# Optimization experiments

Hardware: AMD Instinct MI355X
Metric: run time of the kernel (lower is better)

Reference implementation:

```python
import jax, jax.numpy as jnp
import numpy as np

N_NODES = 50000
N_EDGES = 1600000
IN_C = 64
OUT_C = 64
N_CLASSES = 45


def setup_inputs() -> dict:
    key = jax.random.key(0)
    ks = jax.random.split(key, 12)

    def lin(k, i, o):
        return jax.random.normal(k, (i, o), jnp.float32) / np.float32(np.sqrt(i))

    return dict(
        x=jax.random.normal(ks[0], (N_NODES, IN_C), jnp.float32),
        edge_index=jax.random.randint(ks[1], (2, N_EDGES), 0, N_NODES, dtype=jnp.int32),
        W_z=lin(ks[2], IN_C, OUT_C), b_z=jnp.zeros((OUT_C,), jnp.float32),
        Wl_z=lin(ks[3], 2 * OUT_C, OUT_C), bl_z=jnp.zeros((OUT_C,), jnp.float32),
        W_r=lin(ks[4], IN_C, OUT_C), b_r=jnp.zeros((OUT_C,), jnp.float32),
        Wl_r=lin(ks[5], 2 * OUT_C, OUT_C), bl_r=jnp.zeros((OUT_C,), jnp.float32),
        W_h=lin(ks[6], IN_C, OUT_C), b_h=jnp.zeros((OUT_C,), jnp.float32),
        Wl_h=lin(ks[7], 2 * OUT_C, OUT_C), bl_h=jnp.zeros((OUT_C,), jnp.float32),
        W_out=lin(ks[8], OUT_C, N_CLASSES), b_out=jnp.zeros((N_CLASSES,), jnp.float32),
    )


def _gcn(x, W, b, src, dst, dinv):
    # GCNConv with improved self-loops (fill value 2.0):
    # out = D^{-1/2} (A + 2I) D^{-1/2} X W + b, with deg = in_degree + 2
    xw = x @ W                                   # [N, OUT_C]
    norm = dinv[src] * dinv[dst]                 # [E]
    agg = jax.ops.segment_sum(norm[:, None] * xw[src], dst, num_segments=N_NODES)
    agg = agg + (2.0 * dinv * dinv)[:, None] * xw  # self-loop contribution
    return agg + b


def reference(x, edge_index, W_z, b_z, Wl_z, bl_z, W_r, b_r, Wl_r, bl_r,
              W_h, b_h, Wl_h, bl_h, W_out, b_out):
    src, dst = edge_index[0], edge_index[1]
    deg = jax.ops.segment_sum(jnp.ones((N_EDGES,), jnp.float32), dst,
                              num_segments=N_NODES) + 2.0
    dinv = jax.lax.rsqrt(deg)

    # TGCN cell with H0 = 0 (no prior hidden state passed)
    H = jnp.zeros((N_NODES, OUT_C), x.dtype)
    Z = jax.nn.sigmoid(
        jnp.concatenate([_gcn(x, W_z, b_z, src, dst, dinv), H], axis=1) @ Wl_z + bl_z)
    R = jax.nn.sigmoid(
        jnp.concatenate([_gcn(x, W_r, b_r, src, dst, dinv), H], axis=1) @ Wl_r + bl_r)
    H_tilde = jnp.tanh(
        jnp.concatenate([_gcn(x, W_h, b_h, src, dst, dinv), H * R], axis=1) @ Wl_h + bl_h)
    H = Z * H + (1.0 - Z) * H_tilde

    # relu + linear readout to 45 classes
    return jax.nn.relu(H) @ W_out + b_out
```

## Files before the change

kernel.cpp:

```cpp
#include <hip/hip_runtime.h>

#define N_NODES 50000
#define N_EDGES 1600000
#define NB 782
#define NBB 256
#define CHUNK 6250
#define CAP 2560
#define SCAP 3072
#define ZROW 50000
#define NTILES 3125

typedef unsigned short ushort_t;
typedef _Float16 v8h __attribute__((ext_vector_type(8)));
typedef _Float16 v4h __attribute__((ext_vector_type(4)));
typedef float f32x4_t __attribute__((ext_vector_type(4)));

__global__ __launch_bounds__(256) void k_binw(
    const int* __restrict__ ei, int* __restrict__ gcur, int* __restrict__ bins,
    const float* __restrict__ Wz, const float* __restrict__ bz,
    const float* __restrict__ Wlz, const float* __restrict__ blz,
    const float* __restrict__ Wh, const float* __restrict__ bh,
    const float* __restrict__ Wlh, const float* __restrict__ blh,
    const float* __restrict__ Wout, float* __restrict__ B2f,
    _Float16* __restrict__ Bzh, _Float16* __restrict__ Bwo) {
  __shared__ int arena[8320];
  int tid = threadIdx.x, blk = blockIdx.x;
  if (blk < NBB) {
    int* h    = arena;
    int* segb = arena + NB;
    int* pk   = arena + 2 * NB;
    for (int i = tid; i < NB; i += 256) h[i] = 0;
    __syncthreads();
    const int2* s2 = (const int2*)(ei + blk * CHUNK);
    const int2* d2 = (const int2*)(ei + N_EDGES + blk * CHUNK);
    for (int i = tid; i < CHUNK / 2; i += 256) {
      int2 s = s2[i];
      int2 d = d2[i];
      pk[2 * i]     = s.x | ((d.x & 63) << 16) | ((d.x >> 6) << 22);
      pk[2 * i + 1] = s.y | ((d.y & 63) << 16) | ((d.y >> 6) << 22);
      atomicAdd(&h[d.x >> 6], 1);
      atomicAdd(&h[d.y >> 6], 1);
    }
    __syncthreads();
    for (int b = tid; b < NB; b += 256) {
      int c = h[b];
      segb[b] = c ? atomicAdd(&gcur[b], c) : 0;
      h[b] = 0;
    }
    __syncthreads();
    for (int i = tid; i < CHUNK; i += 256) {
      int v = pk[i];
      int b = (unsigned)v >> 22;
      int p = atomicAdd(&h[b], 1);
      bins[b * CAP + segb[b] + p] = v & 0x3FFFFF;
    }
  } else {
    int wblk = blk - NBB;
    float* A  = (float*)arena;
    float* Bm = (float*)(arena + 4160);
    bool zpath = wblk < 4;
    const float* Wsrc = zpath ? Wz : Wh;
    const float* Lsrc = zpath ? Wlz : Wlh;
    for (int idx = tid; idx < 4096; idx += 256) {
      A[(idx >> 6) * 65 + (idx & 63)] = Wsrc[idx];
      Bm[(idx >> 6) * 65 + (idx & 63)] = Lsrc[idx];
    }
    __syncthreads();
    int lane = (tid >> 1) & 63;
    int j0 = (tid & 1) * 4;
    int ks = (tid >> 7) & 1;
    int k0 = ks * 32 + ((lane >> 4) << 3) + j0;
    int col = (wblk & 3) * 16 + (lane & 15);
    float a0 = 0.f, a1 = 0.f, a2 = 0.f, a3 = 0.f;
    for (int q = 0; q < 64; ++q) {
      float bv = Bm[q * 65 + col];
      a0 = fmaf(A[k0 * 65 + q], bv, a0);
      a1 = fmaf(A[(k0 + 1) * 65 + q], bv, a1);
      a2 = fmaf(A[(k0 + 2) * 65 + q], bv, a2);
      a3 = fmaf(A[(k0 + 3) * 65 + q], bv, a3);
    }
    int tb = wblk * 1024 + tid * 4;
    v4h o; o[0] = (_Float16)a0; o[1] = (_Float16)a1;
    o[2] = (_Float16)a2; o[3] = (_Float16)a3;
    *(v4h*)(Bzh + tb) = o;
    if ((wblk == 0 || wblk == 4) && tid < 64) {
      float v = zpath ? blz[tid] : blh[tid];
      const float* bb = zpath ? bz : bh;
      for (int q = 0; q < 64; ++q) v = fmaf(bb[q], Bm[q * 65 + tid], v);
      B2f[tid * 2 + (zpath ? 0 : 1)] = v;
    }
    if (wblk == 1) {
      for (int e2 = 0; e2 < 12; ++e2) {
        int t2 = tid * 12 + e2;
        int ln = (t2 >> 3) & 63, j = t2 & 7;
        int ntile = t2 >> 10, ks2 = (t2 >> 9) & 1;
        int n = ntile * 16 + (ln & 15);
        int k = ks2 * 32 + ((ln >> 4) << 3) + j;
        Bwo[t2] = (_Float16)((n < 45) ? Wout[k * 45 + n] : 0.f);
      }
    }
  }
}

__global__ __launch_bounds__(256, 4) void k_sort(
    const int* __restrict__ bins, const int* __restrict__ gcur,
    const float* __restrict__ x,
    ushort_t* __restrict__ srcp, int2* __restrict__ rowiv,
    float* __restrict__ dinv, _Float16* __restrict__ xp) {
  __shared__ int dg[64], lo[64], cur[64];
  __shared__ float sdin[64];
  __shared__ int Tsh;
  __shared__ ushort_t buf[8192];
  int tid = threadIdx.x, b = blockIdx.x;
  int start = b * CAP, end = start + gcur[b];
  if (tid < 64) dg[tid] = 0;
  __syncthreads();
  for (int i = start + tid; i < end; i += 256)
    atomicAdd(&dg[bins[i] >> 16], 1);
  __syncthreads();
  int pdv = 0;
  if (tid < 64) { pdv = (dg[tid] + 7) & ~7; lo[tid] = pdv; }
  __syncthreads();
  for (int off = 1; off < 64; off <<= 1) {
    int u = 0;
    if (tid < 64 && tid >= off) u = lo[tid - off];
    __syncthreads();
    if (tid < 64) lo[tid] += u;
    __syncthreads();
  }
  int ex = 0;
  if (tid < 64) {
    ex = lo[tid] - pdv;
    cur[tid] = ex;
    if (tid == 63) Tsh = lo[63];
  }
  __syncthreads();
  int T = Tsh;
  int base = b * SCAP;
  for (int i = tid; i < T; i += 256) buf[i] = (ushort_t)ZROW;
  __syncthreads();
  for (int i = start + tid; i < end; i += 256) {
    int v = bins[i];
    int dl = v >> 16;
    int p = atomicAdd(&cur[dl], 1);
    buf[p] = (ushort_t)(v & 0xFFFF);
  }
  __syncthreads();
  for (int i = tid; i < T; i += 256) srcp[base + i] = buf[i];
  if (tid < 64) {
    int v = b * 64 + tid;
    if (v < N_NODES) {
      rowiv[v] = make_int2(base + ex, pdv);
      float dv = rsqrtf((float)dg[tid] + 2.0f);
      dinv[v] = dv;
      sdin[tid] = dv;
    } else {
      sdin[tid] = 0.f;
    }
  }
  __syncthreads();
  int nb64 = b * 4096;
  for (int idx = tid; idx < 4096; idx += 256) {
    int v = b * 64 + (idx >> 6);
    if (v < N_NODES) xp[nb64 + idx] = (_Float16)(sdin[idx >> 6] * x[nb64 + idx]);
  }
  if (b == 0 && tid < 64) xp[ZROW * 64 + tid] = (_Float16)0.f;
}

__global__ __launch_bounds__(256) void k_agg(
    const ushort_t* __restrict__ srcp, const int2* __restrict__ rowiv,
    const float* __restrict__ dinv, const _Float16* __restrict__ xp,
    _Float16* __restrict__ sxg) {
  int tid = threadIdx.x;
  int lane = tid & 63;
  int grp = lane >> 4;
  int sub = lane & 15;
  int chOff = sub << 2;
  int w = blockIdx.x * 4 + (tid >> 6);
  int nw = gridDim.x * 4;
  for (int v = w; v < N_NODES; v += nw) {
    int vu = __builtin_amdgcn_readfirstlane(v);
    int2 ri = rowiv[vu];
    int beg = ri.x, pd = ri.y;
    float aA0=0.f,aA1=0.f,aA2=0.f,aA3=0.f, aB0=0.f,aB1=0.f,aB2=0.f,aB3=0.f;
    float aC0=0.f,aC1=0.f,aC2=0.f,aC3=0.f, aD0=0.f,aD1=0.f,aD2=0.f,aD3=0.f;
    for (int e = beg; e < beg + pd; e += 64) {
      int rem = beg + pd - e;
      int m = rem < 64 ? rem : 64;
      int sv = (lane < m) ? (int)srcp[e + lane] : ZROW;
      int t = 0;
      for (; t + 16 <= m; t += 16) {
        int sA = __builtin_amdgcn_ds_bpermute((t + grp) << 2, sv);
        int sB = __builtin_amdgcn_ds_bpermute((t + 4 + grp) << 2, sv);
        int sC = __builtin_amdgcn_ds_bpermute((t + 8 + grp) << 2, sv);
        int sD = __builtin_amdgcn_ds_bpermute((t + 12 + grp) << 2, sv);
        v4h rA = *(const v4h*)(xp + (sA << 6) + chOff);
        v4h rB = *(const v4h*)(xp + (sB << 6) + chOff);
        v4h rC = *(const v4h*)(xp + (sC << 6) + chOff);
        v4h rD = *(const v4h*)(xp + (sD << 6) + chOff);
        aA0 += (float)rA[0]; aA1 += (float)rA[1];
        aA2 += (float)rA[2]; aA3 += (float)rA[3];
        aB0 += (float)rB[0]; aB1 += (float)rB[1];
        aB2 += (float)rB[2]; aB3 += (float)rB[3];
        aC0 += (float)rC[0]; aC1 += (float)rC[1];
        aC2 += (float)rC[2]; aC3 += (float)rC[3];
        aD0 += (float)rD[0]; aD1 += (float)rD[1];
        aD2 += (float)rD[2]; aD3 += (float)rD[3];
      }
      if (t < m) {
        int sA = __builtin_amdgcn_ds_bpermute((t + grp) << 2, sv);
        int sB = __builtin_amdgcn_ds_bpermute((t + 4 + grp) << 2, sv);
        v4h rA = *(const v4h*)(xp + (sA << 6) + chOff);
        v4h rB = *(const v4h*)(xp + (sB << 6) + chOff);
        aA0 += (float)rA[0]; aA1 += (float)rA[1];
        aA2 += (float)rA[2]; aA3 += (float)rA[3];
        aB0 += (float)rB[0]; aB1 += (float)rB[1];
        aB2 += (float)rB[2]; aB3 += (float)rB[3];
      }
    }
    float a0 = (aA0 + aB0) + (aC0 + aD0);
    float a1 = (aA1 + aB1) + (aC1 + aD1);
    float a2 = (aA2 + aB2) + (aC2 + aD2);
    float a3 = (aA3 + aB3) + (aC3 + aD3);
    a0 += __shfl_xor(a0, 16); a1 += __shfl_xor(a1, 16);
    a2 += __shfl_xor(a2, 16); a3 += __shfl_xor(a3, 16);
    a0 += __shfl_xor(a0, 32); a1 += __shfl_xor(a1, 32);
    a2 += __shfl_xor(a2, 32); a3 += __shfl_xor(a3, 32);
    if (lane < 16) {
      float dv = dinv[vu];
      v4h self = *(const v4h*)(xp + (vu << 6) + chOff);
      v4h o;
      o[0] = (_Float16)(dv * a0 + 2.f * dv * (float)self[0]);
      o[1] = (_Float16)(dv * a1 + 2.f * dv * (float)self[1]);
      o[2] = (_Float16)(dv * a2 + 2.f * dv * (float)self[2]);
      o[3] = (_Float16)(dv * a3 + 2.f * dv * (float)self[3]);
      *(v4h*)(sxg + (vu << 6) + chOff) = o;
    }
  }
}

__global__ __launch_bounds__(256) void k_cell(
    const _Float16* __restrict__ sxg, const _Float16* __restrict__ Bzh,
    const _Float16* __restrict__ Bwo, const float2* __restrict__ B2,
    const float* __restrict__ bout, float* __restrict__ out) {
  __shared__ __align__(16) _Float16 tbuf[4][16][72];
  int tid = threadIdx.x;
  int lane = tid & 63, wv = tid >> 6;
  int l15 = lane & 15, quad = lane >> 4;
  int tile = blockIdx.x * 4 + wv;
  if (tile >= NTILES) return;

  v8h bzf[8][2], bwf[3][2];
  #pragma unroll
  for (int t = 0; t < 8; ++t)
    #pragma unroll
    for (int ks = 0; ks < 2; ++ks)
      bzf[t][ks] = *(const v8h*)(Bzh + (((t * 2 + ks) * 64 + lane) << 3));
  #pragma unroll
  for (int t = 0; t < 3; ++t)
    #pragma unroll
    for (int ks = 0; ks < 2; ++ks)
      bwf[t][ks] = *(const v8h*)(Bwo + (((t * 2 + ks) * 64 + lane) << 3));
  float zb[4], hb[4], ob[3];
  #pragma unroll
  for (int t = 0; t < 4; ++t) {
    float2 bb = B2[t * 16 + l15];
    zb[t] = bb.x; hb[t] = bb.y;
  }
  #pragma unroll
  for (int t = 0; t < 3; ++t) {
    int c = t * 16 + l15;
    ob[t] = (c < 45) ? bout[c] : 0.f;
  }

  const _Float16* ar = sxg + (tile * 16 + l15) * 64 + quad * 8;
  v8h a0 = *(const v8h*)ar;
  v8h a1 = *(const v8h*)(ar + 32);

  f32x4_t accz[8];
  #pragma unroll
  for (int t = 0; t < 8; ++t) {
    f32x4_t c4 = {0.f, 0.f, 0.f, 0.f};
    c4 = __builtin_amdgcn_mfma_f32_16x16x32_f16(a0, bzf[t][0], c4, 0, 0, 0);
    c4 = __builtin_amdgcn_mfma_f32_16x16x32_f16(a1, bzf[t][1], c4, 0, 0, 0);
    accz[t] = c4;
  }

  #pragma unroll
  for (int t = 0; t < 4; ++t) {
    #pragma unroll
    for (int r = 0; r < 4; ++r) {
      float zv = accz[t][r] + zb[t];
      float hv = accz[t + 4][r] + hb[t];
      float Z = 1.f / (1.f + __expf(-zv));
      float tt = fminf(15.f, fmaxf(-15.f, hv));
      float e2 = __expf(-2.f * tt);
      float Th = (1.f - e2) / (1.f + e2);
      tbuf[wv][quad * 4 + r][t * 16 + l15] = (_Float16)fmaxf((1.f - Z) * Th, 0.f);
    }
  }
  __asm__ volatile("s_waitcnt lgkmcnt(0)" ::: "memory");

  v8h p0 = *(const v8h*)&tbuf[wv][l15][quad * 8];
  v8h p1 = *(const v8h*)&tbuf[wv][l15][32 + quad * 8];

  #pragma unroll
  for (int t = 0; t < 3; ++t) {
    f32x4_t o4 = {0.f, 0.f, 0.f, 0.f};
    o4 = __builtin_amdgcn_mfma_f32_16x16x32_f16(p0, bwf[t][0], o4, 0, 0, 0);
    o4 = __builtin_amdgcn_mfma_f32_16x16x32_f16(p1, bwf[t][1], o4, 0, 0, 0);
    int c = t * 16 + l15;
    if (c < 45) {
      #pragma unroll
      for (int r = 0; r < 4; ++r)
        out[(tile * 16 + quad * 4 + r) * 45 + c] = o4[r] + ob[t];
    }
  }
}

extern "C" void kernel_launch(void* const* d_in, const int* in_sizes, int n_in,
                              void* d_out, int out_size, void* d_ws, size_t ws_size,
                              hipStream_t stream) {
  const float* x    = (const float*)d_in[0];
  const int*   ei   = (const int*)d_in[1];
  const float* Wz   = (const float*)d_in[2];
  const float* bz   = (const float*)d_in[3];
  const float* Wlz  = (const float*)d_in[4];
  const float* blz  = (const float*)d_in[5];
  const float* Wh   = (const float*)d_in[10];
  const float* bh   = (const float*)d_in[11];
  const float* Wlh  = (const float*)d_in[12];
  const float* blh  = (const float*)d_in[13];
  const float* Wout = (const float*)d_in[14];
  const float* bout = (const float*)d_in[15];
  float* out = (float*)d_out;

  char* w = (char*)d_ws;
  int*      bins  = (int*)(w + 0);
  _Float16* sxg   = (_Float16*)(w + 0);
  int*      gcur  = (int*)(w + 8007680);
  ushort_t* srcp  = (ushort_t*)(w + 8010816);
  int2*     rowiv = (int2*)(w + 12815424);
  float*    dinv  = (float*)(w + 13215424);
  float2*   B2    = (float2*)(w + 13415424);
  _Float16* Bzh   = (_Float16*)(w + 13415936);
  _Float16* Bwo   = (_Float16*)(w + 13432320);
  _Float16* xp    = (_Float16*)(w + 13438464);

  hipMemsetAsync(gcur, 0, NB * sizeof(int), stream);
  k_binw <<<NBB + 8, 256, 0, stream>>>(ei, gcur, bins, Wz, bz, Wlz, blz,
                                       Wh, bh, Wlh, blh, Wout,
                                       (float*)B2, Bzh, Bwo);
  k_sort <<<NB, 256, 0, stream>>>(bins, gcur, x, srcp, rowiv, dinv, xp);
  k_agg  <<<2048, 256, 0, stream>>>(srcp, rowiv, dinv, xp, sxg);
  k_cell <<<NB, 256, 0, stream>>>(sxg, Bzh, Bwo, B2, bout, out);
}
```

Baseline: 161.6 us.

## Fuse neighbor aggregation into the GRU cell kernel and vectorize x scaling

```diff
diff --git a/kernel.cpp b/kernel.cpp
--- a/kernel.cpp
+++ b/kernel.cpp
@@ -159,41 +159,68 @@
     }
   }
   __syncthreads();
+  const float4* x4 = (const float4*)x;
+  int base4 = b * 1024;
   int nb64 = b * 4096;
-  for (int idx = tid; idx < 4096; idx += 256) {
-    int v = b * 64 + (idx >> 6);
-    if (v < N_NODES) xp[nb64 + idx] = (_Float16)(sdin[idx >> 6] * x[nb64 + idx]);
+  for (int idx = tid; idx < 1024; idx += 256) {
+    int row = idx >> 4;
+    int v = b * 64 + row;
+    if (v < N_NODES) {
+      float4 xv = x4[base4 + idx];
+      float s = sdin[row];
+      v4h o;
+      o[0] = (_Float16)(s * xv.x); o[1] = (_Float16)(s * xv.y);
+      o[2] = (_Float16)(s * xv.z); o[3] = (_Float16)(s * xv.w);
+      *(v4h*)(xp + nb64 + idx * 4) = o;
+    }
   }
   if (b == 0 && tid < 64) xp[ZROW * 64 + tid] = (_Float16)0.f;
 }
 
-__global__ __launch_bounds__(256) void k_agg(
+__global__ __launch_bounds__(256, 3) void k_aggcell(
     const ushort_t* __restrict__ srcp, const int2* __restrict__ rowiv,
     const float* __restrict__ dinv, const _Float16* __restrict__ xp,
-    _Float16* __restrict__ sxg) {
+    const _Float16* __restrict__ Bzh, const _Float16* __restrict__ Bwo,
+    const float2* __restrict__ B2, const float* __restrict__ bout,
+    float* __restrict__ out) {
+  __shared__ __align__(16) _Float16 sxg_s[4][16][72];
+  __shared__ __align__(16) _Float16 tbuf[4][16][72];
   int tid = threadIdx.x;
-  int lane = tid & 63;
-  int grp = lane >> 4;
-  int sub = lane & 15;
-  int chOff = sub << 2;
-  int w = blockIdx.x * 4 + (tid >> 6);
-  int nw = gridDim.x * 4;
-  for (int v = w; v < N_NODES; v += nw) {
-    int vu = __builtin_amdgcn_readfirstlane(v);
-    int2 ri = rowiv[vu];
-    int beg = ri.x, pd = ri.y;
+  int lane = tid & 63, wv = tid >> 6;
+  int l15 = lane & 15, quad = lane >> 4;
+  int tile = blockIdx.x * 4 + wv;
+  if (tile >= NTILES) return;
+
+  int grp = quad;
+  int chOff = l15 << 2;
+
+  int2 rv = rowiv[tile * 16 + l15];
+  float dvv = dinv[tile * 16 + l15];
+  int beg0 = __shfl(rv.x, 0), pd0 = __shfl(rv.y, 0);
+  int m0 = pd0 < 64 ? pd0 : 64;
+  int sv = (lane < m0) ? (int)srcp[beg0 + lane] : ZROW;
+  for (int i = 0; i < 16; ++i) {
+    int beg = __shfl(rv.x, i), pd = __shfl(rv.y, i);
+    int svc = sv;
+    if (i < 15) {
+      int bn = __shfl(rv.x, i + 1), pn = __shfl(rv.y, i + 1);
+      int mn = pn < 64 ? pn : 64;
+      sv = (lane < mn) ? (int)srcp[bn + lane] : ZROW;
+    }
+    int vu = tile * 16 + i;
+    v4h self = *(const v4h*)(xp + (vu << 6) + chOff);
     float aA0=0.f,aA1=0.f,aA2=0.f,aA3=0.f, aB0=0.f,aB1=0.f,aB2=0.f,aB3=0.f;
     float aC0=0.f,aC1=0.f,aC2=0.f,aC3=0.f, aD0=0.f,aD1=0.f,aD2=0.f,aD3=0.f;
     for (int e = beg; e < beg + pd; e += 64) {
       int rem = beg + pd - e;
       int m = rem < 64 ? rem : 64;
-      int sv = (lane < m) ? (int)srcp[e + lane] : ZROW;
+      int sl = (e == beg) ? svc : ((lane < m) ? (int)srcp[e + lane] : ZROW);
       int t = 0;
       for (; t + 16 <= m; t += 16) {
-        int sA = __builtin_amdgcn_ds_bpermute((t + grp) << 2, sv);
-        int sB = __builtin_amdgcn_ds_bpermute((t + 4 + grp) << 2, sv);
-        int sC = __builtin_amdgcn_ds_bpermute((t + 8 + grp) << 2, sv);
-        int sD = __builtin_amdgcn_ds_bpermute((t + 12 + grp) << 2, sv);
+        int sA = __builtin_amdgcn_ds_bpermute((t + grp) << 2, sl);
+        int sB = __builtin_amdgcn_ds_bpermute((t + 4 + grp) << 2, sl);
+        int sC = __builtin_amdgcn_ds_bpermute((t + 8 + grp) << 2, sl);
+        int sD = __builtin_amdgcn_ds_bpermute((t + 12 + grp) << 2, sl);
         v4h rA = *(const v4h*)(xp + (sA << 6) + chOff);
         v4h rB = *(const v4h*)(xp + (sB << 6) + chOff);
         v4h rC = *(const v4h*)(xp + (sC << 6) + chOff);
@@ -208,8 +235,8 @@
         aD2 += (float)rD[2]; aD3 += (float)rD[3];
       }
       if (t < m) {
-        int sA = __builtin_amdgcn_ds_bpermute((t + grp) << 2, sv);
-        int sB = __builtin_amdgcn_ds_bpermute((t + 4 + grp) << 2, sv);
+        int sA = __builtin_amdgcn_ds_bpermute((t + grp) << 2, sl);
+        int sB = __builtin_amdgcn_ds_bpermute((t + 4 + grp) << 2, sl);
         v4h rA = *(const v4h*)(xp + (sA << 6) + chOff);
         v4h rB = *(const v4h*)(xp + (sB << 6) + chOff);
         aA0 += (float)rA[0]; aA1 += (float)rA[1];
@@ -227,71 +254,35 @@
     a0 += __shfl_xor(a0, 32); a1 += __shfl_xor(a1, 32);
     a2 += __shfl_xor(a2, 32); a3 += __shfl_xor(a3, 32);
     if (lane < 16) {
-      float dv = dinv[vu];
-      v4h self = *(const v4h*)(xp + (vu << 6) + chOff);
+      float dv = __shfl(dvv, i);
       v4h o;
       o[0] = (_Float16)(dv * a0 + 2.f * dv * (float)self[0]);
       o[1] = (_Float16)(dv * a1 + 2.f * dv * (float)self[1]);
       o[2] = (_Float16)(dv * a2 + 2.f * dv * (float)self[2]);
       o[3] = (_Float16)(dv * a3 + 2.f * dv * (float)self[3]);
-      *(v4h*)(sxg + (vu << 6) + chOff) = o;
-    }
-  }
-}
-
-__global__ __launch_bounds__(256) void k_cell(
-    const _Float16* __restrict__ sxg, const _Float16* __restrict__ Bzh,
-    const _Float16* __restrict__ Bwo, const float2* __restrict__ B2,
-    const float* __restrict__ bout, float* __restrict__ out) {
-  __shared__ __align__(16) _Float16 tbuf[4][16][72];
-  int tid = threadIdx.x;
-  int lane = tid & 63, wv = tid >> 6;
-  int l15 = lane & 15, quad = lane >> 4;
-  int tile = blockIdx.x * 4 + wv;
-  if (tile >= NTILES) return;
-
-  v8h bzf[8][2], bwf[3][2];
-  #pragma unroll
-  for (int t = 0; t < 8; ++t)
-    #pragma unroll
-    for (int ks = 0; ks < 2; ++ks)
-      bzf[t][ks] = *(const v8h*)(Bzh + (((t * 2 + ks) * 64 + lane) << 3));
-  #pragma unroll
-  for (int t = 0; t < 3; ++t)
-    #pragma unroll
-    for (int ks = 0; ks < 2; ++ks)
-      bwf[t][ks] = *(const v8h*)(Bwo + (((t * 2 + ks) * 64 + lane) << 3));
-  float zb[4], hb[4], ob[3];
+      *(v4h*)&sxg_s[wv][i][chOff] = o;
+    }
+  }
+  __asm__ volatile("s_waitcnt lgkmcnt(0)" ::: "memory");
+
+  v8h a0f = *(const v8h*)&sxg_s[wv][l15][quad * 8];
+  v8h a1f = *(const v8h*)&sxg_s[wv][l15][32 + quad * 8];
   #pragma unroll
   for (int t = 0; t < 4; ++t) {
+    v8h bz0 = *(const v8h*)(Bzh + (((t * 2 + 0) * 64 + lane) << 3));
+    v8h bz1 = *(const v8h*)(Bzh + (((t * 2 + 1) * 64 + lane) << 3));
+    v8h bh0 = *(const v8h*)(Bzh + ((((t + 4) * 2 + 0) * 64 + lane) << 3));
+    v8h bh1 = *(const v8h*)(Bzh + ((((t + 4) * 2 + 1) * 64 + lane) << 3));
+    f32x4_t cz = {0.f, 0.f, 0.f, 0.f}, chh = {0.f, 0.f, 0.f, 0.f};
+    cz = __builtin_amdgcn_mfma_f32_16x16x32_f16(a0f, bz0, cz, 0, 0, 0);
+    cz = __builtin_amdgcn_mfma_f32_16x16x32_f16(a1f, bz1, cz, 0, 0, 0);
+    chh = __builtin_amdgcn_mfma_f32_16x16x32_f16(a0f, bh0, chh, 0, 0, 0);
+    chh = __builtin_amdgcn_mfma_f32_16x16x32_f16(a1f, bh1, chh, 0, 0, 0);
     float2 bb = B2[t * 16 + l15];
-    zb[t] = bb.x; hb[t] = bb.y;
-  }
-  #pragma unroll
-  for (int t = 0; t < 3; ++t) {
-    int c = t * 16 + l15;
-    ob[t] = (c < 45) ? bout[c] : 0.f;
-  }
-
-  const _Float16* ar = sxg + (tile * 16 + l15) * 64 + quad * 8;
-  v8h a0 = *(const v8h*)ar;
-  v8h a1 = *(const v8h*)(ar + 32);
-
-  f32x4_t accz[8];
-  #pragma unroll
-  for (int t = 0; t < 8; ++t) {
-    f32x4_t c4 = {0.f, 0.f, 0.f, 0.f};
-    c4 = __builtin_amdgcn_mfma_f32_16x16x32_f16(a0, bzf[t][0], c4, 0, 0, 0);
-    c4 = __builtin_amdgcn_mfma_f32_16x16x32_f16(a1, bzf[t][1], c4, 0, 0, 0);
-    accz[t] = c4;
-  }
-
-  #pragma unroll
-  for (int t = 0; t < 4; ++t) {
     #pragma unroll
     for (int r = 0; r < 4; ++r) {
-      float zv = accz[t][r] + zb[t];
-      float hv = accz[t + 4][r] + hb[t];
+      float zv = cz[r] + bb.x;
+      float hv = chh[r] + bb.y;
       float Z = 1.f / (1.f + __expf(-zv));
       float tt = fminf(15.f, fmaxf(-15.f, hv));
       float e2 = __expf(-2.f * tt);
@@ -303,17 +294,19 @@
 
   v8h p0 = *(const v8h*)&tbuf[wv][l15][quad * 8];
   v8h p1 = *(const v8h*)&tbuf[wv][l15][32 + quad * 8];
-
   #pragma unroll
   for (int t = 0; t < 3; ++t) {
+    v8h bw0 = *(const v8h*)(Bwo + (((t * 2 + 0) * 64 + lane) << 3));
+    v8h bw1 = *(const v8h*)(Bwo + (((t * 2 + 1) * 64 + lane) << 3));
     f32x4_t o4 = {0.f, 0.f, 0.f, 0.f};
-    o4 = __builtin_amdgcn_mfma_f32_16x16x32_f16(p0, bwf[t][0], o4, 0, 0, 0);
-    o4 = __builtin_amdgcn_mfma_f32_16x16x32_f16(p1, bwf[t][1], o4, 0, 0, 0);
+    o4 = __builtin_amdgcn_mfma_f32_16x16x32_f16(p0, bw0, o4, 0, 0, 0);
+    o4 = __builtin_amdgcn_mfma_f32_16x16x32_f16(p1, bw1, o4, 0, 0, 0);
     int c = t * 16 + l15;
     if (c < 45) {
+      float obv = bout[c];
       #pragma unroll
       for (int r = 0; r < 4; ++r)
-        out[(tile * 16 + quad * 4 + r) * 45 + c] = o4[r] + ob[t];
+        out[(tile * 16 + quad * 4 + r) * 45 + c] = o4[r] + obv;
     }
   }
 }
@@ -337,7 +330,6 @@
 
   char* w = (char*)d_ws;
   int*      bins  = (int*)(w + 0);
-  _Float16* sxg   = (_Float16*)(w + 0);
   int*      gcur  = (int*)(w + 8007680);
   ushort_t* srcp  = (ushort_t*)(w + 8010816);
   int2*     rowiv = (int2*)(w + 12815424);
@@ -352,6 +344,6 @@
                                        Wh, bh, Wlh, blh, Wout,
                                        (float*)B2, Bzh, Bwo);
   k_sort <<<NB, 256, 0, stream>>>(bins, gcur, x, srcp, rowiv, dinv, xp);
-  k_agg  <<<2048, 256, 0, stream>>>(srcp, rowiv, dinv, xp, sxg);
-  k_cell <<<NB, 256, 0, stream>>>(sxg, Bzh, Bwo, B2, bout, out);
+  k_aggcell <<<NB, 256, 0, stream>>>(srcp, rowiv, dinv, xp, Bzh, Bwo, B2,
+                                     bout, out);
 }
```

New measurement: 167.2 us. +3.5%, slower.
